# Performance work log

Measured on AMD Instinct MI355X. Metric: run time of the kernel, lower is better.

The kernel has to match this reference:

```python
import jax, jax.numpy as jnp
import numpy as np

D = 1024       # nn_embed
I = 512        # ffn_intermediate_size
E = 7          # num routed experts (8 total - 1 shared)
TOPK = 2
B, S = 4, 4096


def setup_inputs() -> dict:
    key = jax.random.key(0)
    ks = jax.random.split(key, 10)
    s = 0.02
    return {
        "x": jax.random.normal(ks[0], (B, S, D), dtype=jnp.float32),
        # shared expert (one): weights stored so y = x @ W
        "sh_gate": jax.random.normal(ks[1], (D, I), dtype=jnp.float32) * s,
        "sh_up":   jax.random.normal(ks[2], (D, I), dtype=jnp.float32) * s,
        "sh_down": jax.random.normal(ks[3], (I, D), dtype=jnp.float32) * s,
        # routed experts stacked [E, ...]
        "r_gate": jax.random.normal(ks[4], (E, D, I), dtype=jnp.float32) * s,
        "r_up":   jax.random.normal(ks[5], (E, D, I), dtype=jnp.float32) * s,
        "r_down": jax.random.normal(ks[6], (E, I, D), dtype=jnp.float32) * s,
        # router linear (has bias in torch) + learnable routing_bias param
        "w_r": jax.random.normal(ks[7], (D, E), dtype=jnp.float32) * s,
        "b_r": jnp.zeros((E,), dtype=jnp.float32),
        "routing_bias": jnp.zeros((E,), dtype=jnp.float32),
    }


def _expert(xt, wg, wu, wd):
    # SwiGLU: down(silu(gate(x)) * up(x))
    return (jax.nn.silu(xt @ wg) * (xt @ wu)) @ wd


def reference(x, sh_gate, sh_up, sh_down, r_gate, r_up, r_down, w_r, b_r, routing_bias):
    Bx, Sx, Dx = x.shape
    T = Bx * Sx
    xt = x.reshape(T, Dx)

    # shared expert (num_shared_experts == 1, no averaging)
    shared_out = _expert(xt, sh_gate, sh_up, sh_down)

    # sigmoid routing with top-k and renormalized combine weights
    logits = xt @ w_r + b_r + routing_bias          # [T, E]
    probs = jax.nn.sigmoid(logits)
    top_p, top_i = jax.lax.top_k(probs, TOPK)       # [T, k]
    top_p = top_p / jnp.sum(top_p, axis=-1, keepdims=True)

    # dense combine-weight matrix: zero where expert not selected
    comb = jnp.zeros((T, E), dtype=x.dtype).at[
        jnp.arange(T)[:, None], top_i].add(top_p)   # [T, E]

    routed_out = jnp.zeros_like(xt)
    for e in range(E):  # small fixed expert count
        y = _expert(xt, r_gate[e], r_up[e], r_down[e])
        routed_out = routed_out + y * comb[:, e:e + 1]

    return (shared_out + routed_out).reshape(Bx, Sx, Dx)
```

## Files before the change

### kernel.cpp

```cpp
#include <hip/hip_runtime.h>
#include <hip/hip_bf16.h>
#include <cstdint>
#include <cstddef>

#define DTOK 1024
#define IFF  512
#define NEXP 7
#define TTOK 16384
#define CAP  (2*TTOK + NEXP*128)
#define CAPX (CAP + TTOK)

typedef __bf16 v8bf  __attribute__((ext_vector_type(8)));
typedef float  f32x4 __attribute__((ext_vector_type(4)));

#define AS1 __attribute__((address_space(1)))
#define AS3 __attribute__((address_space(3)))


__global__ void init_kernel(int* __restrict__ slot_token, float* __restrict__ slot_w,
                            __bf16* __restrict__ zpage) {
    int i = blockIdx.x * 256 + threadIdx.x;
    if (i < CAP) slot_token[i] = -1;
    else if (i < CAPX) { slot_token[i] = i - CAP; slot_w[i] = 1.f; }
    if (i < 512) zpage[i] = (__bf16)0.f;
}

__global__ void cast_x_kernel(const float4* __restrict__ x, __bf16* __restrict__ xb) {
    int i = blockIdx.x * 256 + threadIdx.x;
    float4 v = x[i];
    typedef __bf16 v4bf __attribute__((ext_vector_type(4)));
    v4bf o; o[0] = (__bf16)v.x; o[1] = (__bf16)v.y; o[2] = (__bf16)v.z; o[3] = (__bf16)v.w;
    *reinterpret_cast<v4bf*>(xb + (size_t)i * 4) = o;
}

__global__ __launch_bounds__(256) void build_B1t(
    const float* __restrict__ r_gate, const float* __restrict__ r_up,
    const float* __restrict__ sh_gate, const float* __restrict__ sh_up,
    __bf16* __restrict__ B1) {
    const int kh = blockIdx.x, j = blockIdx.y, e = blockIdx.z;
    const float* G = (e < NEXP) ? (r_gate + (size_t)e * (DTOK * IFF)) : sh_gate;
    const float* U = (e < NEXP) ? (r_up   + (size_t)e * (DTOK * IFF)) : sh_up;
    __shared__ __bf16 lg[16][520];
    __shared__ __bf16 lu[16][520];
    const int tid = threadIdx.x;
    const int c4 = tid & 3, kk0 = tid >> 2;
    #pragma unroll
    for (int p = 0; p < 8; ++p) {
        int kk = kk0 + p * 64;
        size_t off = (size_t)(kh * 512 + kk) * IFF + j * 16 + c4 * 4;
        float4 g = *(const float4*)&G[off];
        float4 u = *(const float4*)&U[off];
        lg[c4*4+0][kk] = (__bf16)g.x; lg[c4*4+1][kk] = (__bf16)g.y;
        lg[c4*4+2][kk] = (__bf16)g.z; lg[c4*4+3][kk] = (__bf16)g.w;
        lu[c4*4+0][kk] = (__bf16)u.x; lu[c4*4+1][kk] = (__bf16)u.y;
        lu[c4*4+2][kk] = (__bf16)u.z; lu[c4*4+3][kk] = (__bf16)u.w;
    }
    __syncthreads();
    const int rr = tid >> 3;
    const int ch0 = tid & 7;
    const int cc = rr & 15;
    const bool isup = rr >= 16;
    const int r = j * 32 + (isup ? 16 : 0) + cc;
    const __bf16* src = isup ? &lu[cc][0] : &lg[cc][0];
    __bf16* dst = B1 + ((size_t)e << 20) + (size_t)r * DTOK + kh * 512;
    #pragma unroll
    for (int q = 0; q < 8; ++q) {
        int ch = ch0 + q * 8;
        *(v8bf*)&dst[ch * 8] = *(const v8bf*)&src[ch * 8];
    }
}

__global__ __launch_bounds__(256) void build_B2t(
    const float* __restrict__ r_down, const float* __restrict__ sh_down,
    __bf16* __restrict__ B2) {
    const int kh = blockIdx.x, nb = blockIdx.y, e = blockIdx.z;
    const float* D = (e < NEXP) ? (r_down + (size_t)e * (IFF * DTOK)) : sh_down;
    __shared__ __bf16 ln[64][264];
    const int tid = threadIdx.x;
    const int c4 = tid & 15, kk0 = tid >> 4;
    #pragma unroll
    for (int p = 0; p < 16; ++p) {
        int kk = kk0 + p * 16;
        size_t off = (size_t)(kh * 256 + kk) * DTOK + nb * 64 + c4 * 4;
        float4 v = *(const float4*)&D[off];
        ln[c4*4+0][kk] = (__bf16)v.x; ln[c4*4+1][kk] = (__bf16)v.y;
        ln[c4*4+2][kk] = (__bf16)v.z; ln[c4*4+3][kk] = (__bf16)v.w;
    }
    __syncthreads();
    const int nn = tid >> 2;
    const int ch0 = tid & 3;
    __bf16* dst = B2 + ((size_t)e * 1024 + nb * 64 + nn) * IFF + kh * 256;
    #pragma unroll
    for (int q = 0; q < 8; ++q) {
        int ch = ch0 + q * 4;
        *(v8bf*)&dst[ch * 8] = *(const v8bf*)&ln[nn][ch * 8];
    }
}

__global__ __launch_bounds__(256) void router_kernel(
    const float* __restrict__ x, const float* __restrict__ w_r,
    const float* __restrict__ b_r, const float* __restrict__ rb,
    int* __restrict__ top_i, float* __restrict__ top_w) {
    int wid = threadIdx.x >> 6, lane = threadIdx.x & 63;
    int t = blockIdx.x * 4 + wid;
    float acc[NEXP] = {0.f,0.f,0.f,0.f,0.f,0.f,0.f};
    #pragma unroll 4
    for (int it = 0; it < DTOK / 64; ++it) {
        int d = it * 64 + lane;
        float xv = x[(size_t)t * DTOK + d];
        const float* wr = w_r + (size_t)d * NEXP;
        #pragma unroll
        for (int e = 0; e < NEXP; ++e) acc[e] += xv * wr[e];
    }
    #pragma unroll
    for (int e = 0; e < NEXP; ++e)
        #pragma unroll
        for (int off = 32; off; off >>= 1) acc[e] += __shfl_xor(acc[e], off);
    if (lane == 0) {
        float p[NEXP];
        #pragma unroll
        for (int e = 0; e < NEXP; ++e) p[e] = 1.f / (1.f + expf(-(acc[e] + b_r[e] + rb[e])));
        int i0 = 0;
        #pragma unroll
        for (int e = 1; e < NEXP; ++e) if (p[e] > p[i0]) i0 = e;
        int i1 = -1;
        #pragma unroll
        for (int e = 0; e < NEXP; ++e) if (e != i0 && (i1 < 0 || p[e] > p[i1])) i1 = e;
        float s = p[i0] + p[i1];
        top_i[2 * t] = i0; top_i[2 * t + 1] = i1;
        top_w[2 * t] = p[i0] / s; top_w[2 * t + 1] = p[i1] / s;
    }
}

__global__ __launch_bounds__(1024) void gather_kernel(
    const int* __restrict__ top_i, const float* __restrict__ top_w,
    int* __restrict__ slot_token, float* __restrict__ slot_w,
    int* __restrict__ tok_slot, int* __restrict__ offs_out) {
    __shared__ int h[NEXP][1024];
    __shared__ int lofs[NEXP];
    const int tid = threadIdx.x;
    const int base = tid * 32;

    int cnt[NEXP] = {0,0,0,0,0,0,0};
    int emem[32];
    float wmem[32];
    #pragma unroll
    for (int j = 0; j < 32; ++j) {
        emem[j] = top_i[base + j];
        wmem[j] = top_w[base + j];
        #pragma unroll
        for (int q = 0; q < NEXP; ++q) if (emem[j] == q) cnt[q]++;
    }
    #pragma unroll
    for (int q = 0; q < NEXP; ++q) h[q][tid] = cnt[q];
    __syncthreads();
    for (int off = 1; off < 1024; off <<= 1) {
        int v[NEXP];
        #pragma unroll
        for (int q = 0; q < NEXP; ++q) v[q] = (tid >= off) ? h[q][tid - off] : 0;
        __syncthreads();
        #pragma unroll
        for (int q = 0; q < NEXP; ++q) h[q][tid] += v[q];
        __syncthreads();
    }
    if (tid == 0) {
        int o = 0;
        #pragma unroll
        for (int q = 0; q < NEXP; ++q) { lofs[q] = o; o += ((h[q][1023] + 127) >> 7) << 7; }
        #pragma unroll
        for (int q = 0; q < NEXP; ++q) offs_out[q] = lofs[q];
        offs_out[NEXP] = CAP;
    }
    __syncthreads();
    int pos[NEXP];
    #pragma unroll
    for (int q = 0; q < NEXP; ++q) pos[q] = lofs[q] + h[q][tid] - cnt[q];
    #pragma unroll
    for (int j = 0; j < 32; ++j) {
        int t = (base + j) >> 1;
        #pragma unroll
        for (int q = 0; q < NEXP; ++q) if (emem[j] == q) {
            slot_token[pos[q]] = t;
            slot_w[pos[q]] = wmem[j];
            tok_slot[base + j] = pos[q];
            pos[q]++;
        }
    }
}

template<int KDIM, int EPI, bool GATHER, typename YT>
__global__ __launch_bounds__(256) void gemm_kernel(
    const __bf16* __restrict__ A, const __bf16* __restrict__ Bmat,
    const int* __restrict__ offs, const int* __restrict__ slot_token,
    const float* __restrict__ slot_w, const int* __restrict__ tok_slot,
    YT* __restrict__ yr,
    __bf16* __restrict__ Hout, float* __restrict__ out,
    const __bf16* __restrict__ zpage) {
    const int nwg = gridDim.x;
    const int cpx = nwg >> 3;
    const int bid = blockIdx.x;
    const int L = (bid & 7) * cpx + (bid >> 3);
    const int tileN = L & 7;
    const int tileM = L >> 3;
    const int tid = threadIdx.x, lane = tid & 63, wid = tid >> 6;
    const int wm = wid >> 1, wn = wid & 1;

    __shared__ __bf16 As[128 * 64];
    __shared__ __bf16 Bs[128 * 64];

    const __bf16* Bp = Bmat;
    if (offs) {
        int m0 = tileM * 128, e = 0;
        #pragma unroll
        for (int i = 1; i < NEXP + 1; ++i) if (m0 >= offs[i]) e = i;
        Bp = Bmat + (size_t)e * (1024 * KDIM);
    }

    f32x4 acc[4][4] = {};

    const int lrow = lane >> 3;
    const int lk = (((lane & 7) ^ lrow) * 8);
    const __bf16* abase[4]; bool apad[4];
    const __bf16* bbase[4];
    #pragma unroll
    for (int i = 0; i < 4; ++i) {
        int ra = tileM * 128 + (wid * 4 + i) * 8 + lrow;
        if (GATHER) {
            int tok = slot_token[ra];
            if (tok >= 0) { abase[i] = A + (size_t)tok * KDIM + lk; apad[i] = false; }
            else          { abase[i] = zpage;                      apad[i] = true;  }
        } else { abase[i] = A + (size_t)ra * KDIM + lk; apad[i] = false; }
        int rb_ = tileN * 128 + (wid * 4 + i) * 8 + lrow;
        bbase[i] = Bp + (size_t)rb_ * KDIM + lk;
    }

    const int swz = (lane & 7) << 3;

    for (int ks = 0; ks < KDIM; ks += 64) {
        #pragma unroll
        for (int i = 0; i < 4; ++i) {
            const __bf16* ga = apad[i] ? abase[i] : (abase[i] + ks);
            __builtin_amdgcn_global_load_lds((const AS1 void*)ga,
                (AS3 void*)&As[(wid * 4 + i) * 512 + lane * 8], 16, 0, 0);
        }
        #pragma unroll
        for (int i = 0; i < 4; ++i) {
            __builtin_amdgcn_global_load_lds((const AS1 void*)(bbase[i] + ks),
                (AS3 void*)&Bs[(wid * 4 + i) * 512 + lane * 8], 16, 0, 0);
        }
        __syncthreads();

        #pragma unroll
        for (int kk = 0; kk < 64; kk += 32) {
            v8bf a[4], b[4];
            int kof = (kk + ((lane >> 4) << 3)) ^ swz;
            int ar = wm * 64 + (lane & 15);
            int br = wn * 64 + (lane & 15);
            #pragma unroll
            for (int mi = 0; mi < 4; ++mi) a[mi] = *reinterpret_cast<const v8bf*>(&As[(ar + mi * 16) * 64 + kof]);
            #pragma unroll
            for (int ni = 0; ni < 4; ++ni) b[ni] = *reinterpret_cast<const v8bf*>(&Bs[(br + ni * 16) * 64 + kof]);
            #pragma unroll
            for (int mi = 0; mi < 4; ++mi)
                #pragma unroll
                for (int ni = 0; ni < 4; ++ni)
                    acc[mi][ni] = __builtin_amdgcn_mfma_f32_16x16x32_bf16(a[mi], b[ni], acc[mi][ni], 0, 0, 0);
        }
        __syncthreads();
    }

    const int mbase = tileM * 128 + wm * 64;
    const int nbase = tileN * 128 + wn * 64;
    const int rowoff = (lane >> 4) * 4;
    const int col = lane & 15;

    if constexpr (EPI == 0) {
        #pragma unroll
        for (int mi = 0; mi < 4; ++mi)
            #pragma unroll
            for (int pi = 0; pi < 2; ++pi) {
                int ni = pi * 2;
                int hcol = (((nbase + ni * 16) >> 5) << 4) + col;
                #pragma unroll
                for (int j = 0; j < 4; ++j) {
                    int m = mbase + mi * 16 + rowoff + j;
                    float g = acc[mi][ni][j];
                    float u = acc[mi][ni + 1][j];
                    float h = (g / (1.f + __expf(-g))) * u;
                    Hout[(size_t)m * IFF + hcol] = (__bf16)h;
                }
            }
    } else if constexpr (EPI == 1) {
        #pragma unroll
        for (int mi = 0; mi < 4; ++mi)
            #pragma unroll
            for (int j = 0; j < 4; ++j) {
                int m = mbase + mi * 16 + rowoff + j;
                #pragma unroll
                for (int ni = 0; ni < 4; ++ni)
                    out[(size_t)m * DTOK + nbase + ni * 16 + col] = acc[mi][ni][j];
            }
    } else if constexpr (EPI == 2) {
        #pragma unroll
        for (int mi = 0; mi < 4; ++mi)
            #pragma unroll
            for (int j = 0; j < 4; ++j) {
                int m = mbase + mi * 16 + rowoff + j;
                if (slot_token[m] < 0) continue;
                float wgt = slot_w[m];
                #pragma unroll
                for (int ni = 0; ni < 4; ++ni)
                    yr[(size_t)m * DTOK + nbase + ni * 16 + col] = (YT)(wgt * acc[mi][ni][j]);
            }
    } else if constexpr (EPI == 3) {
        #pragma unroll
        for (int mi = 0; mi < 4; ++mi)
            #pragma unroll
            for (int j = 0; j < 4; ++j) {
                int m = mbase + mi * 16 + rowoff + j;
                int s0 = tok_slot[2 * m], s1 = tok_slot[2 * m + 1];
                const YT* y0 = yr + (size_t)s0 * DTOK;
                const YT* y1 = yr + (size_t)s1 * DTOK;
                #pragma unroll
                for (int ni = 0; ni < 4; ++ni) {
                    int c = nbase + ni * 16 + col;
                    out[(size_t)m * DTOK + c] = acc[mi][ni][j] + (float)y0[c] + (float)y1[c];
                }
            }
    } else {
        #pragma unroll
        for (int mi = 0; mi < 4; ++mi)
            #pragma unroll
            for (int j = 0; j < 4; ++j) {
                int m = mbase + mi * 16 + rowoff + j;
                int tok = slot_token[m];
                if (tok < 0) continue;
                float wgt = slot_w[m];
                #pragma unroll
                for (int ni = 0; ni < 4; ++ni)
                    atomicAdd(out + (size_t)tok * DTOK + nbase + ni * 16 + col, wgt * acc[mi][ni][j]);
            }
    }
}

extern "C" void kernel_launch(void* const* d_in, const int* in_sizes, int n_in,
                              void* d_out, int out_size, void* d_ws, size_t ws_size,
                              hipStream_t stream) {
    const float* x       = (const float*)d_in[0];
    const float* sh_gate = (const float*)d_in[1];
    const float* sh_up   = (const float*)d_in[2];
    const float* sh_down = (const float*)d_in[3];
    const float* r_gate  = (const float*)d_in[4];
    const float* r_up    = (const float*)d_in[5];
    const float* r_down  = (const float*)d_in[6];
    const float* w_r     = (const float*)d_in[7];
    const float* b_r     = (const float*)d_in[8];
    const float* rb      = (const float*)d_in[9];
    float* out = (float*)d_out;

    char* w = (char*)d_ws;
    __bf16* xb = (__bf16*)w;          w += (size_t)TTOK * DTOK * 2;
    __bf16* B1 = (__bf16*)w;          w += (size_t)8 * 1024 * 1024 * 2;
    __bf16* B2 = (__bf16*)w;          w += (size_t)8 * 1024 * 512 * 2;
    __bf16* H  = (__bf16*)w;          w += (size_t)CAPX * IFF * 2;
    int*    top_i = (int*)w;          w += (size_t)TTOK * 2 * 4;
    float*  top_w = (float*)w;        w += (size_t)TTOK * 2 * 4;
    int*    slot_token = (int*)w;     w += (size_t)CAPX * 4;
    float*  slot_w = (float*)w;       w += (size_t)CAPX * 4;
    int*    tok_slot = (int*)w;       w += (size_t)TTOK * 2 * 4;
    int*    offs = (int*)w;           w += 256;
    __bf16* zpage = (__bf16*)w;       w += 1024;
    void*   Yr = (void*)w;
    size_t used = (size_t)(w - (char*)d_ws);
    size_t rem = (ws_size > used) ? (ws_size - used) : 0;
    bool have_yr = rem >= (size_t)CAP * DTOK * 2;

    init_kernel<<<(CAPX + 255) / 256, 256, 0, stream>>>(slot_token, slot_w, zpage);
    cast_x_kernel<<<(TTOK * DTOK / 4) / 256, 256, 0, stream>>>((const float4*)x, xb);
    build_B1t<<<dim3(2, 32, 8), 256, 0, stream>>>(r_gate, r_up, sh_gate, sh_up, B1);
    build_B2t<<<dim3(2, 16, 8), 256, 0, stream>>>(r_down, sh_down, B2);
    router_kernel<<<TTOK / 4, 256, 0, stream>>>(x, w_r, b_r, rb, top_i, top_w);
    gather_kernel<<<1, 1024, 0, stream>>>(top_i, top_w, slot_token, slot_w, tok_slot, offs);

    dim3 blk(256);
    gemm_kernel<DTOK, 0, true, __bf16><<<(CAPX / 128) * 8, blk, 0, stream>>>(
        xb, B1, offs, slot_token, nullptr, nullptr, nullptr, H, nullptr, zpage);

    if (have_yr) {
        __bf16* yr = (__bf16*)Yr;
        gemm_kernel<IFF, 2, false, __bf16><<<(CAP / 128) * 8, blk, 0, stream>>>(
            H, B2, offs, slot_token, slot_w, nullptr, yr, nullptr, nullptr, zpage);
        gemm_kernel<IFF, 3, false, __bf16><<<(TTOK / 128) * 8, blk, 0, stream>>>(
            H + (size_t)CAP * IFF, B2 + (size_t)NEXP * 1024 * 512,
            nullptr, nullptr, nullptr, tok_slot, yr, nullptr, out, zpage);
    } else {
        gemm_kernel<IFF, 1, false, __bf16><<<(TTOK / 128) * 8, blk, 0, stream>>>(
            H + (size_t)CAP * IFF, B2 + (size_t)NEXP * 1024 * 512,
            nullptr, nullptr, nullptr, nullptr, nullptr, nullptr, out, zpage);
        gemm_kernel<IFF, 4, false, __bf16><<<(CAP / 128) * 8, blk, 0, stream>>>(
            H, B2, offs, slot_token, slot_w, nullptr, nullptr, nullptr, out, zpage);
    }
}
```

Measured before the change: 390.3 us.

## Rewrite grouped GEMM as 256x256 tile, 8-wave, double-buffered pipelined kernel

Replaces the 128x128, 4-wave, single-buffered GEMM with a 256x256, 8-wave (512-thread) kernel. It double-buffers LDS, issues direct global-to-LDS loads two k-steps ahead, and interleaves MFMA quadrants with staging using explicit barriers, waitcnts, sched_barriers and setprio. Expert padding grows to 256 rows and the XCD-aware block remap handles grid sizes not divisible by 8. The aim is more data reuse per tile and overlap of memory latency with matrix math. The cost is extra padded rows, heavy register and LDS use (128KB LDS, 2 blocks per CU requested), and fragile hand scheduling.

```diff
diff --git a/kernel.cpp b/kernel.cpp
--- a/kernel.cpp
+++ b/kernel.cpp
@@ -7,7 +7,7 @@
 #define IFF  512
 #define NEXP 7
 #define TTOK 16384
-#define CAP  (2*TTOK + NEXP*128)
+#define CAP  (2*TTOK + NEXP*256)
 #define CAPX (CAP + TTOK)
 
 typedef __bf16 v8bf  __attribute__((ext_vector_type(8)));
@@ -22,7 +22,7 @@
     int i = blockIdx.x * 256 + threadIdx.x;
     if (i < CAP) slot_token[i] = -1;
     else if (i < CAPX) { slot_token[i] = i - CAP; slot_w[i] = 1.f; }
-    if (i < 512) zpage[i] = (__bf16)0.f;
+    if (i < 2048) zpage[i] = (__bf16)0.f;
 }
 
 __global__ void cast_x_kernel(const float4* __restrict__ x, __bf16* __restrict__ xb) {
@@ -166,7 +166,7 @@
     if (tid == 0) {
         int o = 0;
         #pragma unroll
-        for (int q = 0; q < NEXP; ++q) { lofs[q] = o; o += ((h[q][1023] + 127) >> 7) << 7; }
+        for (int q = 0; q < NEXP; ++q) { lofs[q] = o; o += ((h[q][1023] + 255) >> 8) << 8; }
         #pragma unroll
         for (int q = 0; q < NEXP; ++q) offs_out[q] = lofs[q];
         offs_out[NEXP] = CAP;
@@ -188,95 +188,165 @@
     }
 }
 
+
+#define BARX()  asm volatile("s_barrier" ::: "memory")
+#define LGKM0() do { asm volatile("s_waitcnt lgkmcnt(0)" ::: "memory"); \
+                     __builtin_amdgcn_sched_barrier(0); } while (0)
+#define VMW(n)  do { asm volatile("s_waitcnt vmcnt(" #n ")" ::: "memory"); \
+                     __builtin_amdgcn_sched_barrier(0); } while (0)
+
+#define MMQ(mh, nh)                                                            \
+  do {                                                                         \
+    __builtin_amdgcn_sched_barrier(0);                                         \
+    __builtin_amdgcn_s_setprio(1);                                             \
+    _Pragma("unroll")                                                          \
+    for (int mi = 0; mi < 4; ++mi)                                             \
+      _Pragma("unroll")                                                        \
+      for (int ni = 0; ni < 2; ++ni)                                           \
+        _Pragma("unroll")                                                      \
+        for (int ks = 0; ks < 2; ++ks)                                         \
+          acc[(mh)*4+mi][(nh)*2+ni] = __builtin_amdgcn_mfma_f32_16x16x32_bf16( \
+              afr[(mh)*4+mi][ks], bfr[(nh)*2+ni][ks],                          \
+              acc[(mh)*4+mi][(nh)*2+ni], 0, 0, 0);                             \
+    __builtin_amdgcn_s_setprio(0);                                             \
+    __builtin_amdgcn_sched_barrier(0);                                         \
+  } while (0)
+
+#define STAGE_A(tau, h)                                                        \
+  do {                                                                         \
+    const int _b = (tau) & 1;                                                  \
+    __builtin_amdgcn_global_load_lds((const AS1 void*)(aptr[h][0] + (tau)*64), \
+        (AS3 void*)&As[(_b*2 + (h))*8192 + tid*8], 16, 0, 0);                  \
+    __builtin_amdgcn_global_load_lds((const AS1 void*)(aptr[h][1] + (tau)*64), \
+        (AS3 void*)&As[(_b*2 + (h))*8192 + 4096 + tid*8], 16, 0, 0);           \
+  } while (0)
+
+#define STAGE_B(tau, h)                                                        \
+  do {                                                                         \
+    const int _b = (tau) & 1;                                                  \
+    __builtin_amdgcn_global_load_lds((const AS1 void*)(bptr[h][0] + (tau)*64), \
+        (AS3 void*)&Bs[(_b*2 + (h))*8192 + tid*8], 16, 0, 0);                  \
+    __builtin_amdgcn_global_load_lds((const AS1 void*)(bptr[h][1] + (tau)*64), \
+        (AS3 void*)&Bs[(_b*2 + (h))*8192 + 4096 + tid*8], 16, 0, 0);           \
+  } while (0)
+
 template<int KDIM, int EPI, bool GATHER, typename YT>
-__global__ __launch_bounds__(256) void gemm_kernel(
+__global__ __launch_bounds__(512, 2) void gemm8_kernel(
     const __bf16* __restrict__ A, const __bf16* __restrict__ Bmat,
     const int* __restrict__ offs, const int* __restrict__ slot_token,
     const float* __restrict__ slot_w, const int* __restrict__ tok_slot,
     YT* __restrict__ yr,
     __bf16* __restrict__ Hout, float* __restrict__ out,
     const __bf16* __restrict__ zpage) {
+    constexpr int NKT = KDIM / 64;
     const int nwg = gridDim.x;
-    const int cpx = nwg >> 3;
-    const int bid = blockIdx.x;
-    const int L = (bid & 7) * cpx + (bid >> 3);
-    const int tileN = L & 7;
-    const int tileM = L >> 3;
+    const int q8 = nwg >> 3, r8 = nwg & 7;
+    const int xcd = blockIdx.x & 7, jj = blockIdx.x >> 3;
+    const int L = (xcd < r8 ? xcd * (q8 + 1) : r8 * (q8 + 1) + (xcd - r8) * q8) + jj;
+    const int tileN = L & 3;
+    const int tileM = L >> 2;
     const int tid = threadIdx.x, lane = tid & 63, wid = tid >> 6;
-    const int wm = wid >> 1, wn = wid & 1;
-
-    __shared__ __bf16 As[128 * 64];
-    __shared__ __bf16 Bs[128 * 64];
+    const int wm = wid >> 2, wn = wid & 3;
+
+    __shared__ __bf16 As[2 * 2 * 8192];
+    __shared__ __bf16 Bs[2 * 2 * 8192];
 
     const __bf16* Bp = Bmat;
     if (offs) {
-        int m0 = tileM * 128, e = 0;
+        int m0 = tileM * 256, e = 0;
         #pragma unroll
         for (int i = 1; i < NEXP + 1; ++i) if (m0 >= offs[i]) e = i;
         Bp = Bmat + (size_t)e * (1024 * KDIM);
     }
 
-    f32x4 acc[4][4] = {};
-
-    const int lrow = lane >> 3;
-    const int lk = (((lane & 7) ^ lrow) * 8);
-    const __bf16* abase[4]; bool apad[4];
-    const __bf16* bbase[4];
-    #pragma unroll
-    for (int i = 0; i < 4; ++i) {
-        int ra = tileM * 128 + (wid * 4 + i) * 8 + lrow;
-        if (GATHER) {
-            int tok = slot_token[ra];
-            if (tok >= 0) { abase[i] = A + (size_t)tok * KDIM + lk; apad[i] = false; }
-            else          { abase[i] = zpage;                      apad[i] = true;  }
-        } else { abase[i] = A + (size_t)ra * KDIM + lk; apad[i] = false; }
-        int rb_ = tileN * 128 + (wid * 4 + i) * 8 + lrow;
-        bbase[i] = Bp + (size_t)rb_ * KDIM + lk;
-    }
-
-    const int swz = (lane & 7) << 3;
-
-    for (int ks = 0; ks < KDIM; ks += 64) {
-        #pragma unroll
-        for (int i = 0; i < 4; ++i) {
-            const __bf16* ga = apad[i] ? abase[i] : (abase[i] + ks);
-            __builtin_amdgcn_global_load_lds((const AS1 void*)ga,
-                (AS3 void*)&As[(wid * 4 + i) * 512 + lane * 8], 16, 0, 0);
-        }
-        #pragma unroll
-        for (int i = 0; i < 4; ++i) {
-            __builtin_amdgcn_global_load_lds((const AS1 void*)(bbase[i] + ks),
-                (AS3 void*)&Bs[(wid * 4 + i) * 512 + lane * 8], 16, 0, 0);
-        }
-        __syncthreads();
-
-        #pragma unroll
-        for (int kk = 0; kk < 64; kk += 32) {
-            v8bf a[4], b[4];
-            int kof = (kk + ((lane >> 4) << 3)) ^ swz;
-            int ar = wm * 64 + (lane & 15);
-            int br = wn * 64 + (lane & 15);
-            #pragma unroll
-            for (int mi = 0; mi < 4; ++mi) a[mi] = *reinterpret_cast<const v8bf*>(&As[(ar + mi * 16) * 64 + kof]);
-            #pragma unroll
-            for (int ni = 0; ni < 4; ++ni) b[ni] = *reinterpret_cast<const v8bf*>(&Bs[(br + ni * 16) * 64 + kof]);
-            #pragma unroll
-            for (int mi = 0; mi < 4; ++mi)
-                #pragma unroll
-                for (int ni = 0; ni < 4; ++ni)
-                    acc[mi][ni] = __builtin_amdgcn_mfma_f32_16x16x32_bf16(a[mi], b[ni], acc[mi][ni], 0, 0, 0);
-        }
-        __syncthreads();
-    }
-
-    const int mbase = tileM * 128 + wm * 64;
-    const int nbase = tileN * 128 + wn * 64;
+    const __bf16* aptr[2][2];
+    const __bf16* bptr[2][2];
+    #pragma unroll
+    for (int h = 0; h < 2; ++h)
+        #pragma unroll
+        for (int l = 0; l < 2; ++l) {
+            const int i = tid + l * 512;
+            const int rh = i >> 3;
+            const int swzo = (((tid & 7) ^ (rh & 7)) << 3);
+            const int ra = tileM * 256 + h * 128 + rh;
+            if (GATHER) {
+                int tok = slot_token[ra];
+                aptr[h][l] = (tok >= 0 ? A + (size_t)tok * KDIM : zpage) + swzo;
+            } else {
+                aptr[h][l] = A + (size_t)ra * KDIM + swzo;
+            }
+            const int rbg = tileN * 256 + h * 128 + rh;
+            bptr[h][l] = Bp + (size_t)rbg * KDIM + swzo;
+        }
+
+    const int kko0 = (((lane >> 4) ^ (lane & 7)) << 3);
+    const int kko1 = (((4 + (lane >> 4)) ^ (lane & 7)) << 3);
+    const int arow = (lane & 15) * 64;
+    const int abase0 = (0 * 2 + wm) * 8192 + arow;
+    const int abase1 = (1 * 2 + wm) * 8192 + arow;
+    const int bbase0 = (0 * 2 + (wn >> 1)) * 8192 + (wn & 1) * 4096 + arow;
+    const int bbase1 = (1 * 2 + (wn >> 1)) * 8192 + (wn & 1) * 4096 + arow;
+
+    f32x4 acc[8][4] = {};
+    v8bf afr[8][2], bfr[4][2];
+
+    STAGE_B(0, 0); STAGE_B(0, 1); STAGE_A(0, 0); STAGE_A(0, 1);
+    STAGE_B(1, 0); STAGE_B(1, 1); STAGE_A(1, 0);
+    VMW(6);
+    BARX();
+
+    #pragma unroll 2
+    for (int t = 0; t < NKT; ++t) {
+        const int ab = ((t & 1) ? abase1 : abase0);
+        const int bb = ((t & 1) ? bbase1 : bbase0);
+        #pragma unroll
+        for (int mi = 0; mi < 4; ++mi) {
+            afr[mi][0] = *(const v8bf*)&As[ab + mi * 1024 + kko0];
+            afr[mi][1] = *(const v8bf*)&As[ab + mi * 1024 + kko1];
+        }
+        #pragma unroll
+        for (int ni = 0; ni < 4; ++ni) {
+            bfr[ni][0] = *(const v8bf*)&Bs[bb + ni * 1024 + kko0];
+            bfr[ni][1] = *(const v8bf*)&Bs[bb + ni * 1024 + kko1];
+        }
+        if (t + 1 < NKT) STAGE_A(t + 1, 1);
+        BARX();
+        LGKM0();
+        MMQ(0, 0);
+        BARX();
+        #pragma unroll
+        for (int mi = 4; mi < 8; ++mi) {
+            afr[mi][0] = *(const v8bf*)&As[ab + mi * 1024 + kko0];
+            afr[mi][1] = *(const v8bf*)&As[ab + mi * 1024 + kko1];
+        }
+        if (t + 2 < NKT) STAGE_B(t + 2, 0);
+        BARX();
+        LGKM0();
+        MMQ(1, 0);
+        BARX();
+        if (t + 2 < NKT) STAGE_B(t + 2, 1);
+        BARX();
+        MMQ(0, 1);
+        BARX();
+        if (t + 2 < NKT) {
+            STAGE_A(t + 2, 0);
+            VMW(6);
+        } else if (t + 1 < NKT) {
+            VMW(0);
+        }
+        BARX();
+        MMQ(1, 1);
+        BARX();
+    }
+
+    const int mbase = tileM * 256 + wm * 128;
+    const int nbase = tileN * 256 + wn * 64;
     const int rowoff = (lane >> 4) * 4;
     const int col = lane & 15;
 
     if constexpr (EPI == 0) {
         #pragma unroll
-        for (int mi = 0; mi < 4; ++mi)
+        for (int mi = 0; mi < 8; ++mi)
             #pragma unroll
             for (int pi = 0; pi < 2; ++pi) {
                 int ni = pi * 2;
@@ -292,7 +362,7 @@
             }
     } else if constexpr (EPI == 1) {
         #pragma unroll
-        for (int mi = 0; mi < 4; ++mi)
+        for (int mi = 0; mi < 8; ++mi)
             #pragma unroll
             for (int j = 0; j < 4; ++j) {
                 int m = mbase + mi * 16 + rowoff + j;
@@ -302,7 +372,7 @@
             }
     } else if constexpr (EPI == 2) {
         #pragma unroll
-        for (int mi = 0; mi < 4; ++mi)
+        for (int mi = 0; mi < 8; ++mi)
             #pragma unroll
             for (int j = 0; j < 4; ++j) {
                 int m = mbase + mi * 16 + rowoff + j;
@@ -314,7 +384,7 @@
             }
     } else if constexpr (EPI == 3) {
         #pragma unroll
-        for (int mi = 0; mi < 4; ++mi)
+        for (int mi = 0; mi < 8; ++mi)
             #pragma unroll
             for (int j = 0; j < 4; ++j) {
                 int m = mbase + mi * 16 + rowoff + j;
@@ -329,7 +399,7 @@
             }
     } else {
         #pragma unroll
-        for (int mi = 0; mi < 4; ++mi)
+        for (int mi = 0; mi < 8; ++mi)
             #pragma unroll
             for (int j = 0; j < 4; ++j) {
                 int m = mbase + mi * 16 + rowoff + j;
@@ -369,7 +439,7 @@
     float*  slot_w = (float*)w;       w += (size_t)CAPX * 4;
     int*    tok_slot = (int*)w;       w += (size_t)TTOK * 2 * 4;
     int*    offs = (int*)w;           w += 256;
-    __bf16* zpage = (__bf16*)w;       w += 1024;
+    __bf16* zpage = (__bf16*)w;       w += 4096;
     void*   Yr = (void*)w;
     size_t used = (size_t)(w - (char*)d_ws);
     size_t rem = (ws_size > used) ? (ws_size - used) : 0;
@@ -382,22 +452,22 @@
     router_kernel<<<TTOK / 4, 256, 0, stream>>>(x, w_r, b_r, rb, top_i, top_w);
     gather_kernel<<<1, 1024, 0, stream>>>(top_i, top_w, slot_token, slot_w, tok_slot, offs);
 
-    dim3 blk(256);
-    gemm_kernel<DTOK, 0, true, __bf16><<<(CAPX / 128) * 8, blk, 0, stream>>>(
+    dim3 blk(512);
+    gemm8_kernel<DTOK, 0, true, __bf16><<<(CAPX / 256) * 4, blk, 0, stream>>>(
         xb, B1, offs, slot_token, nullptr, nullptr, nullptr, H, nullptr, zpage);
 
     if (have_yr) {
         __bf16* yr = (__bf16*)Yr;
-        gemm_kernel<IFF, 2, false, __bf16><<<(CAP / 128) * 8, blk, 0, stream>>>(
+        gemm8_kernel<IFF, 2, false, __bf16><<<(CAP / 256) * 4, blk, 0, stream>>>(
             H, B2, offs, slot_token, slot_w, nullptr, yr, nullptr, nullptr, zpage);
-        gemm_kernel<IFF, 3, false, __bf16><<<(TTOK / 128) * 8, blk, 0, stream>>>(
+        gemm8_kernel<IFF, 3, false, __bf16><<<(TTOK / 256) * 4, blk, 0, stream>>>(
             H + (size_t)CAP * IFF, B2 + (size_t)NEXP * 1024 * 512,
             nullptr, nullptr, nullptr, tok_slot, yr, nullptr, out, zpage);
     } else {
-        gemm_kernel<IFF, 1, false, __bf16><<<(TTOK / 128) * 8, blk, 0, stream>>>(
+        gemm8_kernel<IFF, 1, false, __bf16><<<(TTOK / 256) * 4, blk, 0, stream>>>(
             H + (size_t)CAP * IFF, B2 + (size_t)NEXP * 1024 * 512,
             nullptr, nullptr, nullptr, nullptr, nullptr, nullptr, out, zpage);
-        gemm_kernel<IFF, 4, false, __bf16><<<(CAP / 128) * 8, blk, 0, stream>>>(
+        gemm8_kernel<IFF, 4, false, __bf16><<<(CAP / 256) * 4, blk, 0, stream>>>(
             H, B2, offs, slot_token, slot_w, nullptr, nullptr, nullptr, out, zpage);
     }
 }
```

Result: slower. 518.1 us (+32.8%).
